# Kernel optimization log

Hardware: AMD Instinct MI355X
Metric: run time of the kernel (lower is better)

The kernel has to match this reference:

```python
import jax, jax.numpy as jnp
import numpy as np

T, B, C, H, W = 8, 16, 384, 32, 32
HEADS, CHUNK = 8, 2
EPS = 1e-5


def setup_inputs() -> dict:
    key = jax.random.key(0)
    ks = jax.random.split(key, 6)
    s = 1.0 / np.sqrt(C)
    bn = jnp.stack([jnp.ones(C), jnp.zeros(C), jnp.zeros(C), jnp.ones(C)])  # gamma,beta,mean,var
    return {
        'x': jax.random.normal(ks[0], (T, B, C, H, W), jnp.float32),
        'q_w': jax.random.normal(ks[1], (C, C), jnp.float32) * s,
        'q_bn': bn,
        'k_w': jax.random.normal(ks[2], (C, C), jnp.float32) * s,
        'k_bn': bn,
        'v_w': jax.random.normal(ks[3], (C, C), jnp.float32) * s,
        'v_bn': bn,
        'proj_w': jax.random.normal(ks[4], (C, C), jnp.float32) * s,
        'proj_b': jnp.zeros((C,), jnp.float32),
        'proj_bn': bn,
    }


def _conv1x1(x, w, b=None):
    # x: [T,B,C,H,W], w: [Cout,Cin]
    y = jnp.einsum('tbchw,oc->tbohw', x, w)
    if b is not None:
        y = y + b[None, None, :, None, None]
    return y


def _bn(x, p):
    g, b, m, v = p  # each [C]
    inv = g * jax.lax.rsqrt(v + EPS)
    return x * inv[None, None, :, None, None] + (b - m * inv)[None, None, :, None, None]


def _heads(x):
    # [T,B,C,H,W] -> [T,B,heads,N,hd]
    hd = C // HEADS
    return x.reshape(T, B, HEADS, hd, H * W).transpose(0, 1, 2, 4, 3)


def reference(x, q_w, q_bn, k_w, k_bn, v_w, v_bn, proj_w, proj_b, proj_bn):
    hd = C // HEADS
    N = H * W
    nc = T // CHUNK
    identity = x
    xs = jax.nn.relu(x)  # shortcut_lif -> ReLU (use_snn=False)

    q = _heads(jax.nn.relu(_bn(_conv1x1(xs, q_w), q_bn)))
    k = _heads(jax.nn.relu(_bn(_conv1x1(xs, k_w), k_bn)))
    v = _heads(jax.nn.relu(_bn(_conv1x1(xs, v_w), v_bn)))

    def chunkify(t):  # [T,B,h,N,d] -> [nc,B,h,CHUNK*N,d]
        return t.reshape(nc, CHUNK, B, HEADS, N, hd).transpose(0, 2, 3, 1, 4, 5).reshape(nc, B, HEADS, CHUNK * N, hd)

    qc, kc, vc = chunkify(q), chunkify(k), chunkify(v)
    scale = 1.0 / H  # non-dvs scaling
    attn = jnp.einsum('cbhsd,cbhse->cbhde', kc, vc) * scale  # [nc,B,h,d,d]
    out = jnp.einsum('cbhsd,cbhde->cbhse', qc, attn)          # [nc,B,h,S,d]

    out = out.reshape(nc, B, HEADS, CHUNK, N, hd).transpose(0, 3, 1, 2, 4, 5).reshape(T, B, HEADS, N, hd)
    y = out.transpose(0, 1, 2, 4, 3).reshape(T, B, C, N)  # merge heads back to channels
    y = jax.nn.relu(y).reshape(T, B, C, H, W)  # attn_lif -> ReLU
    y = _bn(_conv1x1(y, proj_w, proj_b), proj_bn)
    y = y + identity
    return (y, v)
```

## Files before the change

kernel.cpp:

```cpp
#include <hip/hip_runtime.h>

typedef unsigned short u16;
typedef unsigned long long u64;
typedef float f32x4 __attribute__((ext_vector_type(4)));
typedef __bf16 bf16x8 __attribute__((ext_vector_type(8)));

#define T_ 8
#define B_ 16
#define C_ 384
#define N_ 1024
#define HEADS_ 8
#define HD_ 48
#define NC_ 4
#define EPS_ 1e-5f
#define SCALE_ (1.0f / 32.0f)

__device__ __forceinline__ float bf2f(u16 u) {
  union { unsigned int i; float f; } x;
  x.i = ((unsigned int)u) << 16;
  return x.f;
}
__device__ __forceinline__ u16 f2bf(float f) {
  unsigned int u = __float_as_uint(f);
  u += 0x7fffu + ((u >> 16) & 1u);
  return (u16)(u >> 16);
}

__device__ __forceinline__ void glds16(const void* g, void* s) {
  __builtin_amdgcn_global_load_lds(
      (const __attribute__((address_space(1))) void*)g,
      (__attribute__((address_space(3))) void*)s, 16, 0, 0);
}

__global__ __launch_bounds__(256) void wconv(const float* __restrict__ a,
                                             const float* __restrict__ b,
                                             const float* __restrict__ c,
                                             const float* __restrict__ d,
                                             u16* __restrict__ o) {
  const int m = blockIdx.x / 72;
  const float* s = (m == 0) ? a : (m == 1) ? b : (m == 2) ? c : d;
  const size_t off = (size_t)(blockIdx.x % 72) * 2048 + (size_t)threadIdx.x * 8;
  float4 f0 = *(const float4*)(s + off);
  float4 f1 = *(const float4*)(s + off + 4);
  u16 h[8] = {f2bf(f0.x), f2bf(f0.y), f2bf(f0.z), f2bf(f0.w),
              f2bf(f1.x), f2bf(f1.y), f2bf(f1.z), f2bf(f1.w)};
  *(uint4*)(o + (size_t)m * (C_ * C_) + off) = *(const uint4*)h;
}

__global__ __launch_bounds__(256) void prep_xt(const float* __restrict__ x,
                                               u16* __restrict__ xt) {
  const int tb = blockIdx.y;
  const int n = blockIdx.x * 64 + (threadIdx.x & 63);
  const int cg = threadIdx.x >> 6;
  const float* xb = x + (size_t)tb * C_ * N_ + n;
  u16* ob = xt + ((size_t)tb * N_ + n) * C_;
#pragma unroll
  for (int g = 0; g < 12; ++g) {
    int c = (cg + g * 4) * 8;
    u16 h[8];
#pragma unroll
    for (int j = 0; j < 8; ++j)
      h[j] = f2bf(fmaxf(xb[(size_t)(c + j) * N_], 0.f));
    *(uint4*)(ob + c) = *(const uint4*)h;
  }
}

__global__ __launch_bounds__(256) void qkv_gemm(
    const u16* __restrict__ xt, const u16* __restrict__ wbf,
    const float* __restrict__ bnq, const float* __restrict__ bnk,
    const float* __restrict__ bnv,
    u16* __restrict__ qo, u16* __restrict__ ko, float* __restrict__ vo) {
  const int tb = blockIdx.z / 3;
  const int pr = blockIdx.z % 3;
  const int n0 = blockIdx.x * 128;
  const int o0 = blockIdx.y * 128;
  const float* bn = (pr == 0) ? bnq : (pr == 1) ? bnk : bnv;
  const u16* wp = wbf + (size_t)pr * (C_ * C_);
  const u16* xb = xt + (size_t)tb * N_ * C_;

  __shared__ u16 As[2 * 128 * 64];
  __shared__ u16 Bs[2 * 128 * 64];

  const int tid = threadIdx.x;
  const int lane = tid & 63;
  const int wave = tid >> 6;
  const int wr = wave >> 1, wc = wave & 1;
  const int qd = lane >> 4, l15 = lane & 15;

  f32x4 acc[4][4];
#pragma unroll
  for (int i = 0; i < 4; ++i)
#pragma unroll
    for (int j = 0; j < 4; ++j) acc[i][j] = (f32x4){0.f, 0.f, 0.f, 0.f};

  auto stage = [&](int buf, int c0) {
#pragma unroll
    for (int i = 0; i < 4; ++i) {
      const int L = i * 256 + tid;
      const int row = L >> 3;
      const int g = (L & 7) ^ (row & 7);
      glds16(wp + (size_t)(o0 + row) * C_ + c0 + g * 8,
             As + (size_t)buf * (128 * 64) + (size_t)(i * 256 + wave * 64) * 8);
      glds16(xb + (size_t)(n0 + row) * C_ + c0 + g * 8,
             Bs + (size_t)buf * (128 * 64) + (size_t)(i * 256 + wave * 64) * 8);
    }
  };

  stage(0, 0);
  __syncthreads();

  for (int s = 0; s < 6; ++s) {
    const int cur = s & 1;
    if (s < 5) {
      stage(cur ^ 1, (s + 1) * 64);
      __builtin_amdgcn_sched_barrier(0);
    }
    const u16* Ac = As + cur * (128 * 64);
    const u16* Bc = Bs + cur * (128 * 64);
#pragma unroll
    for (int kk = 0; kk < 2; ++kk) {
      bf16x8 wf[4], xf[4];
#pragma unroll
      for (int mi = 0; mi < 4; ++mi) {
        int r = wr * 64 + mi * 16 + l15;
        wf[mi] = *(const bf16x8*)(Ac + r * 64 + (((kk * 4 + qd) ^ (r & 7)) * 8));
      }
#pragma unroll
      for (int ni = 0; ni < 4; ++ni) {
        int r = wc * 64 + ni * 16 + l15;
        xf[ni] = *(const bf16x8*)(Bc + r * 64 + (((kk * 4 + qd) ^ (r & 7)) * 8));
      }
      if (pr != 2) {
#pragma unroll
        for (int mi = 0; mi < 4; ++mi)
#pragma unroll
          for (int ni = 0; ni < 4; ++ni)
            acc[mi][ni] = __builtin_amdgcn_mfma_f32_16x16x32_bf16(
                wf[mi], xf[ni], acc[mi][ni], 0, 0, 0);
      } else {
#pragma unroll
        for (int ni = 0; ni < 4; ++ni)
#pragma unroll
          for (int mi = 0; mi < 4; ++mi)
            acc[ni][mi] = __builtin_amdgcn_mfma_f32_16x16x32_bf16(
                xf[ni], wf[mi], acc[ni][mi], 0, 0, 0);
      }
    }
    __syncthreads();
  }

  if (pr < 2) {
    u16* out = (pr == 0) ? qo : ko;
#pragma unroll
    for (int mi = 0; mi < 4; ++mi) {
#pragma unroll
      for (int r = 0; r < 4; ++r) {
        int o = o0 + wr * 64 + mi * 16 + qd * 4 + r;
        float inv = bn[o] * rsqrtf(bn[3 * C_ + o] + EPS_);
        float sh = bn[C_ + o] - bn[2 * C_ + o] * inv;
        size_t rowbase = ((size_t)tb * C_ + o) * N_;
#pragma unroll
        for (int ni = 0; ni < 4; ++ni) {
          int n = n0 + wc * 64 + ni * 16 + l15;
          out[rowbase + n] = f2bf(fmaxf(acc[mi][ni][r] * inv + sh, 0.f));
        }
      }
    }
  } else {
#pragma unroll
    for (int bj = 0; bj < 4; ++bj) {
      int o = o0 + wr * 64 + bj * 16 + l15;
      float inv = bn[o] * rsqrtf(bn[3 * C_ + o] + EPS_);
      float sh = bn[C_ + o] - bn[2 * C_ + o] * inv;
      int hh = o / HD_, dd = o % HD_;
      size_t base = (((size_t)tb * HEADS_ + hh) * N_) * HD_ + dd;
#pragma unroll
      for (int ai = 0; ai < 4; ++ai)
#pragma unroll
        for (int r = 0; r < 4; ++r) {
          int n = n0 + wc * 64 + ai * 16 + qd * 4 + r;
          vo[base + (size_t)n * HD_] = fmaxf(acc[ai][bj][r] * inv + sh, 0.f);
        }
    }
  }
}

__global__ __launch_bounds__(256) void attn_kv(const u16* __restrict__ kk,
                                               const float* __restrict__ vv,
                                               float* __restrict__ part) {
  const int g2 = blockIdx.x;
  const int tc = g2 & 1;
  const int g = g2 >> 1;
  const int h = g & (HEADS_ - 1);
  const int b = (g >> 3) & (B_ - 1);
  const int cI = g >> 7;
  const int t = cI * 2 + tc;
  const int tid = threadIdx.x;
  const int lane = tid & 63;
  const int wave = tid >> 6;
  const int qd = lane >> 4, l15 = lane & 15;

  __shared__ u16 Ks[2][48 * 128];
  __shared__ u16 Vt[2][48 * 128];

  const size_t kbase = ((size_t)(t * B_ + b) * C_ + h * HD_) * N_;
  const size_t vbase = ((size_t)(t * B_ + b) * HEADS_ + h) * (size_t)N_ * HD_;
  const int ksc = (tid & 15) ^ ((tid >> 4) & 7);

  f32x4 acc[3][3];
#pragma unroll
  for (int m = 0; m < 3; ++m)
#pragma unroll
    for (int n = 0; n < 3; ++n) acc[m][n] = (f32x4){0.f, 0.f, 0.f, 0.f};

  float4 va[3], vb[3];

  auto issue_v = [&](int sb) {
    size_t nb = (size_t)sb * 128;
#pragma unroll
    for (int i = 0; i < 3; ++i) {
      const float* p = vv + vbase + (nb + 2 * lane) * HD_ + (i * 4 + wave) * 4;
      va[i] = *(const float4*)p;
      vb[i] = *(const float4*)(p + HD_);
    }
  };
  auto issue_k = [&](int sb, int bf) {
    size_t nb = (size_t)sb * 128;
#pragma unroll
    for (int i = 0; i < 3; ++i)
      glds16(kk + kbase + (size_t)(i * 16 + (tid >> 4)) * N_ + nb + ksc * 8,
             &Ks[bf][(i * 256 + wave * 64) * 8]);
  };
  auto write_vt = [&](int bf) {
    unsigned* vt = (unsigned*)Vt[bf];
#pragma unroll
    for (int i = 0; i < 3; ++i) {
      int eq = i * 4 + wave;
      const float* fa = (const float*)&va[i];
      const float* fb = (const float*)&vb[i];
#pragma unroll
      for (int j = 0; j < 4; ++j) {
        int e = eq * 4 + j;
        unsigned pk = (unsigned)f2bf(fa[j]) | ((unsigned)f2bf(fb[j]) << 16);
        vt[e * 64 + (((lane >> 2) ^ (e & 7)) << 2) + (lane & 3)] = pk;
      }
    }
  };

  issue_v(0);
  __builtin_amdgcn_sched_barrier(0);
  issue_k(0, 0);
  __builtin_amdgcn_sched_barrier(0);
  write_vt(0);
  __syncthreads();

  for (int sb = 0; sb < 8; ++sb) {
    const int cur = sb & 1;
    if (sb < 7) {
      issue_v(sb + 1);
      __builtin_amdgcn_sched_barrier(0);
      issue_k(sb + 1, cur ^ 1);
      __builtin_amdgcn_sched_barrier(0);
    }
    const u16* kc = Ks[cur];
    const u16* vc = Vt[cur];
    bf16x8 af[3], bfv[3];
#pragma unroll
    for (int m = 0; m < 3; ++m) {
      int d = m * 16 + l15;
      af[m] =
          *(const bf16x8*)(kc + d * 128 + (((wave * 4 + qd) ^ (d & 7)) << 3));
    }
#pragma unroll
    for (int n = 0; n < 3; ++n) {
      int e = n * 16 + l15;
      bfv[n] =
          *(const bf16x8*)(vc + e * 128 + (((wave * 4 + qd) ^ (e & 7)) << 3));
    }
#pragma unroll
    for (int m = 0; m < 3; ++m)
#pragma unroll
      for (int n = 0; n < 3; ++n)
        acc[m][n] = __builtin_amdgcn_mfma_f32_16x16x32_bf16(af[m], bfv[n],
                                                            acc[m][n], 0, 0, 0);
    if (sb < 7) write_vt(cur ^ 1);
    __syncthreads();
  }

  float* red = (float*)&Ks[0][0];
  if (wave >= 2) {
    float* dst = red + (wave - 2) * 2304;
#pragma unroll
    for (int m = 0; m < 3; ++m)
#pragma unroll
      for (int n = 0; n < 3; ++n)
#pragma unroll
        for (int r = 0; r < 4; ++r)
          dst[((m * 3 + n) * 4 + r) * 64 + lane] = acc[m][n][r];
  }
  __syncthreads();
  if (wave < 2) {
    const float* sp = red + wave * 2304;
#pragma unroll
    for (int m = 0; m < 3; ++m)
#pragma unroll
      for (int n = 0; n < 3; ++n)
#pragma unroll
        for (int r = 0; r < 4; ++r)
          acc[m][n][r] += sp[((m * 3 + n) * 4 + r) * 64 + lane];
  }
  __syncthreads();
  if (wave == 1) {
#pragma unroll
    for (int m = 0; m < 3; ++m)
#pragma unroll
      for (int n = 0; n < 3; ++n)
#pragma unroll
        for (int r = 0; r < 4; ++r)
          red[((m * 3 + n) * 4 + r) * 64 + lane] = acc[m][n][r];
  }
  __syncthreads();
  if (wave == 0) {
#pragma unroll
    for (int m = 0; m < 3; ++m)
#pragma unroll
      for (int n = 0; n < 3; ++n)
#pragma unroll
        for (int r = 0; r < 4; ++r) {
          float v = acc[m][n][r] + red[((m * 3 + n) * 4 + r) * 64 + lane];
          int d = m * 16 + qd * 4 + r;
          int e = n * 16 + l15;
          part[(size_t)g2 * 2304 + d * 48 + e] = v * SCALE_;
        }
  }
}

__global__ __launch_bounds__(256) void q_attn(const u16* __restrict__ qq,
                                              const float* __restrict__ part,
                                              u16* __restrict__ aot) {
  const int n0 = blockIdx.x * 64;
  const int z = blockIdx.y;
  const int h = z % HEADS_;
  const int b = (z / HEADS_) % B_;
  const int t = z / (HEADS_ * B_);
  const int cI = t / 2;
  const int g = (cI * B_ + b) * HEADS_ + h;
  const int tid = threadIdx.x;
  const int nl = tid & 63, eg = tid >> 6, e0 = eg * 12;

  __shared__ float at[48 * 48];
  for (int idx = tid; idx < 48 * 48; idx += 256)
    at[idx] = part[(size_t)(g * 2) * 2304 + idx] +
              part[(size_t)(g * 2 + 1) * 2304 + idx];
  __syncthreads();

  size_t qbase = ((size_t)(t * B_ + b) * C_ + h * HD_) * N_ + n0 + nl;
  float acc[12];
#pragma unroll
  for (int j = 0; j < 12; ++j) acc[j] = 0.f;
  for (int d = 0; d < 48; ++d) {
    float qv = bf2f(qq[qbase + (size_t)d * N_]);
#pragma unroll
    for (int j = 0; j < 12; ++j) acc[j] += qv * at[d * 48 + e0 + j];
  }
  u16 hb[12];
#pragma unroll
  for (int j = 0; j < 12; ++j) hb[j] = f2bf(fmaxf(acc[j], 0.f));
  u16* op = aot + ((size_t)(t * B_ + b) * N_ + n0 + nl) * C_ + h * HD_ + e0;
  const u64* hp = (const u64*)hb;
#pragma unroll
  for (int j = 0; j < 3; ++j) ((u64*)op)[j] = hp[j];
}

__global__ __launch_bounds__(256) void proj_gemm(
    const u16* __restrict__ aot, const u16* __restrict__ pwbf,
    const float* __restrict__ pb, const float* __restrict__ pbn,
    const float* __restrict__ x, float* __restrict__ y) {
  const int tb = blockIdx.z;
  const int n0 = blockIdx.x * 128;
  const int o0 = blockIdx.y * 128;
  const u16* ab = aot + (size_t)tb * N_ * C_;

  __shared__ u16 As[2 * 128 * 64];
  __shared__ u16 Bs[2 * 128 * 64];

  const int tid = threadIdx.x;
  const int lane = tid & 63;
  const int wave = tid >> 6;
  const int wr = wave >> 1, wc = wave & 1;
  const int qd = lane >> 4, l15 = lane & 15;

  f32x4 acc[4][4];
#pragma unroll
  for (int i = 0; i < 4; ++i)
#pragma unroll
    for (int j = 0; j < 4; ++j) acc[i][j] = (f32x4){0.f, 0.f, 0.f, 0.f};

  auto stage = [&](int buf, int c0) {
#pragma unroll
    for (int i = 0; i < 4; ++i) {
      const int L = i * 256 + tid;
      const int row = L >> 3;
      const int g = (L & 7) ^ (row & 7);
      glds16(pwbf + (size_t)(o0 + row) * C_ + c0 + g * 8,
             As + (size_t)buf * (128 * 64) + (size_t)(i * 256 + wave * 64) * 8);
      glds16(ab + (size_t)(n0 + row) * C_ + c0 + g * 8,
             Bs + (size_t)buf * (128 * 64) + (size_t)(i * 256 + wave * 64) * 8);
    }
  };

  stage(0, 0);
  __syncthreads();

  for (int s = 0; s < 6; ++s) {
    const int cur = s & 1;
    if (s < 5) {
      stage(cur ^ 1, (s + 1) * 64);
      __builtin_amdgcn_sched_barrier(0);
    }
    const u16* Ac = As + cur * (128 * 64);
    const u16* Bc = Bs + cur * (128 * 64);
#pragma unroll
    for (int kk = 0; kk < 2; ++kk) {
      bf16x8 wf[4], xf[4];
#pragma unroll
      for (int mi = 0; mi < 4; ++mi) {
        int r = wr * 64 + mi * 16 + l15;
        wf[mi] = *(const bf16x8*)(Ac + r * 64 + (((kk * 4 + qd) ^ (r & 7)) * 8));
      }
#pragma unroll
      for (int ni = 0; ni < 4; ++ni) {
        int r = wc * 64 + ni * 16 + l15;
        xf[ni] = *(const bf16x8*)(Bc + r * 64 + (((kk * 4 + qd) ^ (r & 7)) * 8));
      }
#pragma unroll
      for (int mi = 0; mi < 4; ++mi)
#pragma unroll
        for (int ni = 0; ni < 4; ++ni)
          acc[mi][ni] = __builtin_amdgcn_mfma_f32_16x16x32_bf16(
              wf[mi], xf[ni], acc[mi][ni], 0, 0, 0);
    }
    __syncthreads();
  }

#pragma unroll
  for (int mi = 0; mi < 4; ++mi) {
#pragma unroll
    for (int r = 0; r < 4; ++r) {
      int o = o0 + wr * 64 + mi * 16 + qd * 4 + r;
      float g = pbn[o], be = pbn[C_ + o];
      float mu = pbn[2 * C_ + o], va = pbn[3 * C_ + o];
      float inv = g * rsqrtf(va + EPS_);
      float add = pb[o] * inv + (be - mu * inv);
      size_t rowbase = ((size_t)tb * C_ + o) * N_;
#pragma unroll
      for (int ni = 0; ni < 4; ++ni) {
        int n = n0 + wc * 64 + ni * 16 + l15;
        float val = acc[mi][ni][r] * inv + add;
        val += x[rowbase + n];
        y[rowbase + n] = val;
      }
    }
  }
}

extern "C" void kernel_launch(void* const* d_in, const int* in_sizes, int n_in,
                              void* d_out, int out_size, void* d_ws,
                              size_t ws_size, hipStream_t stream) {
  const float* x = (const float*)d_in[0];
  const float* q_w = (const float*)d_in[1];
  const float* q_bn = (const float*)d_in[2];
  const float* k_w = (const float*)d_in[3];
  const float* k_bn = (const float*)d_in[4];
  const float* v_w = (const float*)d_in[5];
  const float* v_bn = (const float*)d_in[6];
  const float* p_w = (const float*)d_in[7];
  const float* p_b = (const float*)d_in[8];
  const float* p_bn = (const float*)d_in[9];

  const size_t NELEM = (size_t)T_ * B_ * C_ * N_;
  float* y_out = (float*)d_out;
  float* v_out = y_out + NELEM;

  u16* q_ws = (u16*)y_out;
  u16* xt_ws = q_ws + NELEM;
  float* part_ws = (float*)xt_ws;
  u16* k_ws = (u16*)d_ws;
  u16* wbf = k_ws + NELEM;
  u16* ao_ws = k_ws;

  wconv<<<dim3(288), 256, 0, stream>>>(q_w, k_w, v_w, p_w, wbf);
  prep_xt<<<dim3(16, 128), 256, 0, stream>>>(x, xt_ws);
  qkv_gemm<<<dim3(8, 3, T_ * B_ * 3), 256, 0, stream>>>(
      xt_ws, wbf, q_bn, k_bn, v_bn, q_ws, k_ws, v_out);
  attn_kv<<<dim3(NC_ * B_ * HEADS_ * 2), 256, 0, stream>>>(k_ws, v_out,
                                                           part_ws);
  q_attn<<<dim3(16, T_ * B_ * HEADS_), 256, 0, stream>>>(q_ws, part_ws, ao_ws);
  proj_gemm<<<dim3(8, 3, T_ * B_), 256, 0, stream>>>(
      ao_ws, wbf + 3 * C_ * C_, p_b, p_bn, x, y_out);
}
```

Before: 1.178 ms.

## Replace double-buffered LDS staging with single-buffer loop in QKV and proj GEMMs

Both GEMM kernels drop their double-buffered shared-memory prefetch and switch to a single buffer per operand, with a barrier before and after each K-slice load. This halves LDS usage from 64KB to 32KB per block, which may let more blocks share a CU. In exchange, global-to-LDS loads no longer overlap with the MFMA work of the previous slice, and there is an extra barrier per iteration.

```diff
diff --git a/kernel.cpp b/kernel.cpp
--- a/kernel.cpp
+++ b/kernel.cpp
@@ -78,8 +78,8 @@
   const u16* wp = wbf + (size_t)pr * (C_ * C_);
   const u16* xb = xt + (size_t)tb * N_ * C_;
 
-  __shared__ u16 As[2 * 128 * 64];
-  __shared__ u16 Bs[2 * 128 * 64];
+  __shared__ u16 As[128 * 64];
+  __shared__ u16 Bs[128 * 64];
 
   const int tid = threadIdx.x;
   const int lane = tid & 63;
@@ -93,42 +93,31 @@
 #pragma unroll
     for (int j = 0; j < 4; ++j) acc[i][j] = (f32x4){0.f, 0.f, 0.f, 0.f};
 
-  auto stage = [&](int buf, int c0) {
+  for (int c0 = 0; c0 < C_; c0 += 64) {
+    __syncthreads();
 #pragma unroll
     for (int i = 0; i < 4; ++i) {
       const int L = i * 256 + tid;
       const int row = L >> 3;
       const int g = (L & 7) ^ (row & 7);
       glds16(wp + (size_t)(o0 + row) * C_ + c0 + g * 8,
-             As + (size_t)buf * (128 * 64) + (size_t)(i * 256 + wave * 64) * 8);
+             As + (size_t)(i * 256 + wave * 64) * 8);
       glds16(xb + (size_t)(n0 + row) * C_ + c0 + g * 8,
-             Bs + (size_t)buf * (128 * 64) + (size_t)(i * 256 + wave * 64) * 8);
-    }
-  };
-
-  stage(0, 0);
-  __syncthreads();
-
-  for (int s = 0; s < 6; ++s) {
-    const int cur = s & 1;
-    if (s < 5) {
-      stage(cur ^ 1, (s + 1) * 64);
-      __builtin_amdgcn_sched_barrier(0);
-    }
-    const u16* Ac = As + cur * (128 * 64);
-    const u16* Bc = Bs + cur * (128 * 64);
+             Bs + (size_t)(i * 256 + wave * 64) * 8);
+    }
+    __syncthreads();
 #pragma unroll
     for (int kk = 0; kk < 2; ++kk) {
       bf16x8 wf[4], xf[4];
 #pragma unroll
       for (int mi = 0; mi < 4; ++mi) {
         int r = wr * 64 + mi * 16 + l15;
-        wf[mi] = *(const bf16x8*)(Ac + r * 64 + (((kk * 4 + qd) ^ (r & 7)) * 8));
+        wf[mi] = *(const bf16x8*)(As + r * 64 + (((kk * 4 + qd) ^ (r & 7)) * 8));
       }
 #pragma unroll
       for (int ni = 0; ni < 4; ++ni) {
         int r = wc * 64 + ni * 16 + l15;
-        xf[ni] = *(const bf16x8*)(Bc + r * 64 + (((kk * 4 + qd) ^ (r & 7)) * 8));
+        xf[ni] = *(const bf16x8*)(Bs + r * 64 + (((kk * 4 + qd) ^ (r & 7)) * 8));
       }
       if (pr != 2) {
 #pragma unroll
@@ -146,7 +135,6 @@
                 xf[ni], wf[mi], acc[ni][mi], 0, 0, 0);
       }
     }
-    __syncthreads();
   }
 
   if (pr < 2) {
@@ -381,8 +369,8 @@
   const int o0 = blockIdx.y * 128;
   const u16* ab = aot + (size_t)tb * N_ * C_;
 
-  __shared__ u16 As[2 * 128 * 64];
-  __shared__ u16 Bs[2 * 128 * 64];
+  __shared__ u16 As[128 * 64];
+  __shared__ u16 Bs[128 * 64];
 
   const int tid = threadIdx.x;
   const int lane = tid & 63;
@@ -396,42 +384,31 @@
 #pragma unroll
     for (int j = 0; j < 4; ++j) acc[i][j] = (f32x4){0.f, 0.f, 0.f, 0.f};
 
-  auto stage = [&](int buf, int c0) {
+  for (int c0 = 0; c0 < C_; c0 += 64) {
+    __syncthreads();
 #pragma unroll
     for (int i = 0; i < 4; ++i) {
       const int L = i * 256 + tid;
       const int row = L >> 3;
       const int g = (L & 7) ^ (row & 7);
       glds16(pwbf + (size_t)(o0 + row) * C_ + c0 + g * 8,
-             As + (size_t)buf * (128 * 64) + (size_t)(i * 256 + wave * 64) * 8);
+             As + (size_t)(i * 256 + wave * 64) * 8);
       glds16(ab + (size_t)(n0 + row) * C_ + c0 + g * 8,
-             Bs + (size_t)buf * (128 * 64) + (size_t)(i * 256 + wave * 64) * 8);
-    }
-  };
-
-  stage(0, 0);
-  __syncthreads();
-
-  for (int s = 0; s < 6; ++s) {
-    const int cur = s & 1;
-    if (s < 5) {
-      stage(cur ^ 1, (s + 1) * 64);
-      __builtin_amdgcn_sched_barrier(0);
-    }
-    const u16* Ac = As + cur * (128 * 64);
-    const u16* Bc = Bs + cur * (128 * 64);
+             Bs + (size_t)(i * 256 + wave * 64) * 8);
+    }
+    __syncthreads();
 #pragma unroll
     for (int kk = 0; kk < 2; ++kk) {
       bf16x8 wf[4], xf[4];
 #pragma unroll
       for (int mi = 0; mi < 4; ++mi) {
         int r = wr * 64 + mi * 16 + l15;
-        wf[mi] = *(const bf16x8*)(Ac + r * 64 + (((kk * 4 + qd) ^ (r & 7)) * 8));
+        wf[mi] = *(const bf16x8*)(As + r * 64 + (((kk * 4 + qd) ^ (r & 7)) * 8));
       }
 #pragma unroll
       for (int ni = 0; ni < 4; ++ni) {
         int r = wc * 64 + ni * 16 + l15;
-        xf[ni] = *(const bf16x8*)(Bc + r * 64 + (((kk * 4 + qd) ^ (r & 7)) * 8));
+        xf[ni] = *(const bf16x8*)(Bs + r * 64 + (((kk * 4 + qd) ^ (r & 7)) * 8));
       }
 #pragma unroll
       for (int mi = 0; mi < 4; ++mi)
@@ -440,7 +417,6 @@
           acc[mi][ni] = __builtin_amdgcn_mfma_f32_16x16x32_bf16(
               wf[mi], xf[ni], acc[mi][ni], 0, 0, 0);
     }
-    __syncthreads();
   }
 
 #pragma unroll
```

Result: faster. 1.091 ms (-7.4%).
